# Optimization experiments

Hardware: AMD Instinct MI355X
Metric: run time of the kernel (lower is better)

Reference implementation:

```python
import jax, jax.numpy as jnp
import numpy as np

THR = 10.0           # spike threshold (all layers, igarss2023 config)
LEAK1, LEAK2, LEAK3 = 9.0, 1.0, 0.0  # subtractive leak per layer
POOL1_K, POOL1_S = 7, 6
POOL2_K, POOL2_S = 2, 2
WTA_BLOCK = 2        # local spatial WTA window


def conv2d_same(x, w):
    # x: (B,C,H,W), w: (O,I,kh,kw)
    return jax.lax.conv_general_dilated(
        x, w, window_strides=(1, 1), padding='SAME',
        dimension_numbers=('NCHW', 'OIHW', 'NCHW'))


def maxpool(x, k, s):
    return jax.lax.reduce_window(
        x, -jnp.inf, jax.lax.max, (1, 1, k, k), (1, 1, s, s), 'VALID')


def wta(mem, spk, block=WTA_BLOCK):
    """Winner-take-all lateral inhibition ('both' mode):
    (1) channel competition: only the channel with max membrane at each
        spatial location may spike; (2) local spatial competition: only the
        max-membrane neuron within each block x block window of each map
        may spike. Requires H,W divisible by block."""
    C = mem.shape[1]
    ch_win = jnp.argmax(mem, axis=1)                         # (B,H,W)
    ch_mask = jax.nn.one_hot(ch_win, C, axis=1, dtype=mem.dtype)  # (B,C,H,W)
    loc = jax.lax.reduce_window(
        mem, -jnp.inf, jax.lax.max,
        (1, 1, block, block), (1, 1, block, block), 'VALID')
    loc_up = jnp.repeat(jnp.repeat(loc, block, axis=2), block, axis=3)
    sp_mask = (mem >= loc_up).astype(mem.dtype)
    return spk * ch_mask * sp_mask


def lif_step(mem, inp, leak, use_wta):
    # integrate -> threshold -> WTA -> reset-to-zero -> subtractive leak
    mem = mem + inp
    spk = (mem >= THR).astype(mem.dtype)
    if use_wta:
        spk = wta(mem, spk)
    mem = jnp.where(spk > 0, 0.0, mem)
    mem = jnp.maximum(mem - leak, 0.0)
    return mem, spk


def setup_inputs() -> dict:
    key = jax.random.key(0)
    k0, k1, k2, k3 = jax.random.split(key, 4)
    T, B, H, W = 20, 8, 256, 256
    x = jax.random.uniform(k0, (T, B, 1, H, W), dtype=jnp.float32)
    # STDP-style weights are non-negative in [0,1)
    w1 = jax.random.uniform(k1, (4, 1, 5, 5), dtype=jnp.float32)
    w2 = jax.random.uniform(k2, (36, 4, 5, 5), dtype=jnp.float32)
    w3 = jax.random.uniform(k3, (1, 36, 7, 7), dtype=jnp.float32)
    return {"x": x, "w1": w1, "w2": w2, "w3": w3}


def reference(x, w1, w2, w3):
    T, B, _, H, W = x.shape
    H1, W1 = H, W                                   # conv1 SAME
    H2 = (H1 - POOL1_K) // POOL1_S + 1              # 42
    W2 = (W1 - POOL1_K) // POOL1_S + 1
    H3 = (H2 - POOL2_K) // POOL2_S + 1              # 21
    W3 = (W2 - POOL2_K) // POOL2_S + 1
    C1, C2, C3 = w1.shape[0], w2.shape[0], w3.shape[0]

    m1_0 = jnp.zeros((B, C1, H1, W1), x.dtype)
    m2_0 = jnp.zeros((B, C2, H2, W2), x.dtype)
    m3_0 = jnp.zeros((B, C3, H3, W3), x.dtype)

    def step(carry, xt):
        m1, m2, m3 = carry
        m1, s1 = lif_step(m1, conv2d_same(xt, w1), LEAK1, True)
        p1 = maxpool(s1, POOL1_K, POOL1_S)
        m2, s2 = lif_step(m2, conv2d_same(p1, w2), LEAK2, True)
        p2 = maxpool(s2, POOL2_K, POOL2_S)
        m3, s3 = lif_step(m3, conv2d_same(p2, w3), LEAK3, False)
        return (m1, m2, m3), s3

    _, cls_spikes = jax.lax.scan(step, (m1_0, m2_0, m3_0), x)
    return cls_spikes  # (T, B, n_classes, H3, W3)
```

## Files before the change

### kernel.cpp

```cpp
#include <hip/hip_runtime.h>
#include <stdint.h>

#define THR 10.0f
#define AGT __HIP_MEMORY_SCOPE_AGENT

static constexpr size_t OFF_P2  = 2097152;
static constexpr size_t OFF_BAR = 2359296;

static __device__ __forceinline__ uint64_t ldu64(const uint64_t* p) {
    return __hip_atomic_load(p, __ATOMIC_RELAXED, AGT);
}
static __device__ __forceinline__ void stu64(uint64_t* p, uint64_t v) {
    __hip_atomic_store(p, v, __ATOMIC_RELAXED, AGT);
}

__global__ __launch_bounds__(256) void zero_bar(uint32_t* __restrict__ bar) {
    if (threadIdx.x < 256) bar[threadIdx.x] = 0u;
}

__device__ __forceinline__ void gbar(uint32_t* bar, int bid, uint32_t n) {
    __syncthreads();
    if (threadIdx.x == 0) {
        uint32_t* base = bar + (bid >> 6) * 32;
        uint32_t a = __hip_atomic_fetch_add(base, 1u, __ATOMIC_RELAXED, AGT);
        if (a == 64u * n - 1u)
            __hip_atomic_fetch_add(base + 16, 1u, __ATOMIC_RELAXED, AGT);
        while (__hip_atomic_load(base + 16, __ATOMIC_RELAXED, AGT) < n)
            __builtin_amdgcn_s_sleep(2);
    }
    __syncthreads();
}

__global__ __launch_bounds__(256, 2) void spike_persist(
    const float* __restrict__ x,
    const float* __restrict__ w1,
    const float* __restrict__ w2,
    const float* __restrict__ w3,
    float* __restrict__ out,
    uint8_t* __restrict__ s1b,
    uint8_t* __restrict__ p2b,
    uint32_t* __restrict__ bar)
{
    __shared__ union {
        float    xs[2112];
        uint64_t st64[279];
    } u;
    __shared__ float    ps[400];
    __shared__ float    mem_s[1296];
    __shared__ float    bm_s[324];
    __shared__ int      wc_s[36];
    __shared__ uint32_t p2a[18];

    const int tid = threadIdx.x;
    const int bid = blockIdx.x;
    uint32_t nbar = 0;

    const int b1 = bid >> 6;
    const int r0 = (bid & 63) * 4;
    const int tr = tid >> 7, tc = tid & 127;

    const int tIdx = bid & 63;
    const int b2 = bid >> 6;
    const int tyi = tIdx >> 3, txi = tIdx & 7;
    const int oy2 = tyi < 5 ? 6 * tyi : 30 + 4 * (tyi - 5);
    const int ox2 = txi < 5 ? 6 * txi : 30 + 4 * (txi - 5);
    const int th2 = tyi < 5 ? 6 : 4;
    const int tw2 = txi < 5 ? 6 : 4;
    const int wave = tid >> 6, lane = tid & 63;
    const int pr = lane / 6, pc = lane - 6 * pr;
    const bool act = (pr < th2) && (pc < tw2);
    const int prA = pr > 5 ? 0 : pr, pcA = pc;

    const int lid3 = (bid & 63) * 4 + wave;
    const int kyl = lane / 7, kxl = lane % 7;

    float w3v[36];
#pragma unroll
    for (int c = 0; c < 36; c++) w3v[c] = (lane < 49) ? w3[c * 49 + lane] : 0.f;

    int aoff[9]; uint32_t avalm = 0;
#pragma unroll
    for (int i = 0; i < 9; i++) {
        int idx = tid + i * 256;
        int row = idx / 264, col = idx - row * 264;
        int gy = r0 + row - 2, gx = col - 2;
        if ((idx < 2112) && gy >= 0 && gy < 256 && gx >= 0 && gx < 256)
            avalm |= 1u << i;
        aoff[i] = gy * 256 + gx;
    }
    const int s1soff64 = (b1 * 128 + (r0 >> 1) + tr) * 32 + (tc >> 2);

    const int rb0 = 3 * oy2 - 6;
    const int cb0 = (3 * ox2 - 6) >> 1;
    const int cq0 = cb0 >> 1;
    const int d16 = 2 * (cb0 & 1);
    int boff[2]; uint32_t bvalm = 0;
#pragma unroll
    for (int i = 0; i < 2; i++) {
        int idx = tid + i * 256;
        int row = idx / 9, q = idx - 9 * row;
        int grow = rb0 + row;
        int ucol = 2 * (cq0 + q);
        if ((idx < 279) && grow >= 0 && grow < 128 && ucol >= 0 && ucol < 64)
            bvalm |= 1u << i;
        boff[i] = (b2 * 128 + grow) * 32 + cq0 + q;
    }

    bool l3in[2], l3v[2]; int l3o[2];
#pragma unroll
    for (int rep = 0; rep < 2; rep++) {
        int o = lid3 + rep * 256;
        int rr = o / 21, cl = o - rr * 21;
        int yy = rr + kyl - 3, xx = cl + kxl - 3;
        l3in[rep] = o < 441;
        l3v[rep] = (o < 441) && (lane < 49) && yy >= 0 && yy < 21 && xx >= 0 && xx < 21;
        l3o[rep] = b2 * 441 + yy * 21 + xx;
    }

    float m1r[4][2][2];
#pragma unroll
    for (int c = 0; c < 4; c++)
#pragma unroll
        for (int dy = 0; dy < 2; dy++)
#pragma unroll
            for (int dx = 0; dx < 2; dx++) m1r[c][dy][dx] = 0.f;
    float m2r[9];
#pragma unroll
    for (int i = 0; i < 9; i++) m2r[i] = 0.f;
    float m3r[2] = {0.f, 0.f};

    for (int k = 0; k < 7; k++) {
        for (int tt = 0; tt < 4; tt++) {
            const int t = 4 * k + tt;
            if (t < 20) {
                uint64_t* s1w = reinterpret_cast<uint64_t*>(s1b + (size_t)(t & 7) * 262144);
                const float* xb = x + ((size_t)t * 8 + b1) * 65536;
                __syncthreads();
#pragma unroll
                for (int i = 0; i < 9; i++) {
                    int idx = tid + i * 256;
                    if (idx < 2112) u.xs[idx] = ((avalm >> i) & 1u) ? xb[aoff[i]] : 0.f;
                }
                __syncthreads();

                const float2* xs2 = reinterpret_cast<const float2*>(u.xs);
                float p[6][6];
#pragma unroll
                for (int i = 0; i < 6; i++)
#pragma unroll
                    for (int j = 0; j < 3; j++) {
                        float2 v = xs2[(2 * tr + i) * 132 + tc + j];
                        p[i][2 * j] = v.x; p[i][2 * j + 1] = v.y;
                    }

                float acc[4][2][2];
#pragma unroll
                for (int c = 0; c < 4; c++)
#pragma unroll
                    for (int dy = 0; dy < 2; dy++)
#pragma unroll
                        for (int dx = 0; dx < 2; dx++) acc[c][dy][dx] = 0.f;
#pragma unroll
                for (int c = 0; c < 4; c++)
#pragma unroll
                    for (int ky = 0; ky < 5; ky++)
#pragma unroll
                        for (int kx = 0; kx < 5; kx++) {
                            float w = w1[c * 25 + ky * 5 + kx];
#pragma unroll
                            for (int dy = 0; dy < 2; dy++)
#pragma unroll
                                for (int dx = 0; dx < 2; dx++)
                                    acc[c][dy][dx] = fmaf(p[dy + ky][dx + kx], w, acc[c][dy][dx]);
                        }

                float mem[4][2][2];
#pragma unroll
                for (int c = 0; c < 4; c++)
#pragma unroll
                    for (int dy = 0; dy < 2; dy++)
#pragma unroll
                        for (int dx = 0; dx < 2; dx++)
                            mem[c][dy][dx] = m1r[c][dy][dx] + acc[c][dy][dx];

                int wc[2][2];
#pragma unroll
                for (int dy = 0; dy < 2; dy++)
#pragma unroll
                    for (int dx = 0; dx < 2; dx++) {
                        int w = 0; float mx = mem[0][dy][dx];
#pragma unroll
                        for (int c = 1; c < 4; c++) {
                            float v = mem[c][dy][dx];
                            if (v > mx) { mx = v; w = c; }
                        }
                        wc[dy][dx] = w;
                    }

                float bm[4];
#pragma unroll
                for (int c = 0; c < 4; c++)
                    bm[c] = fmaxf(fmaxf(mem[c][0][0], mem[c][0][1]),
                                  fmaxf(mem[c][1][0], mem[c][1][1]));

                uint32_t bits = 0;
#pragma unroll
                for (int c = 0; c < 4; c++)
#pragma unroll
                    for (int dy = 0; dy < 2; dy++)
#pragma unroll
                        for (int dx = 0; dx < 2; dx++) {
                            float m = mem[c][dy][dx];
                            bool s = (m >= THR) && (wc[dy][dx] == c) && (m >= bm[c]);
                            m1r[c][dy][dx] = fmaxf((s ? 0.f : m) - 9.0f, 0.f);
                            bits |= (s ? 1u : 0u) << (c * 4 + dy * 2 + dx);
                        }
                uint32_t b32 = bits | ((uint32_t)__shfl_xor((int)bits, 1, 64) << 16);
                uint64_t b64 = (uint64_t)b32 |
                               ((uint64_t)(uint32_t)__shfl_xor((int)b32, 2, 64) << 32);
                if (!(tid & 3)) stu64(s1w + s1soff64, b64);
            }
        }

        for (int tt = 0; tt < 4; tt++) {
            const int tl = 4 * k - 8 + tt;
            if (tl >= 0 && tl < 20) {
                const uint64_t* pb64 = reinterpret_cast<const uint64_t*>(
                    p2b + (size_t)(tl & 7) * 32768);
#pragma unroll
                for (int rep = 0; rep < 2; rep++) {
                    if (l3in[rep]) {
                        int o = lid3 + rep * 256;
                        uint64_t v = l3v[rep] ? ldu64(pb64 + l3o[rep]) : 0ull;
                        uint32_t lo = (uint32_t)v, hi = (uint32_t)(v >> 32);
                        float accv = 0.f;
#pragma unroll
                        for (int c = 0; c < 32; c++) accv += ((lo >> c) & 1u) ? w3v[c] : 0.f;
#pragma unroll
                        for (int c = 0; c < 4; c++)  accv += ((hi >> c) & 1u) ? w3v[32 + c] : 0.f;
#pragma unroll
                        for (int off = 32; off; off >>= 1) accv += __shfl_xor(accv, off, 64);
                        float memv3 = m3r[rep] + accv;
                        bool s = memv3 >= THR;
                        if (lane == 0) out[(size_t)tl * 3528 + b2 * 441 + o] = s ? 1.f : 0.f;
                        m3r[rep] = fmaxf(s ? 0.f : memv3, 0.f);
                    }
                }
            }
        }

        for (int tt = 0; tt < 4; tt++) {
            const int tb = 4 * k - 4 + tt;
            if (tb >= 0 && tb < 20) {
                const uint64_t* s1r64 = reinterpret_cast<const uint64_t*>(
                    s1b + (size_t)(tb & 7) * 262144);
                uint64_t* p2w64 = reinterpret_cast<uint64_t*>(p2b + (size_t)(tb & 7) * 32768);

                __syncthreads();
#pragma unroll
                for (int i = 0; i < 2; i++) {
                    int idx = tid + i * 256;
                    if (idx < 279)
                        u.st64[idx] = ((bvalm >> i) & 1u) ? ldu64(s1r64 + boff[i]) : 0ull;
                }
                if (tid < 18) p2a[tid] = 0;
                __syncthreads();

                if (tid < 100) {
                    int r = tid / 10, cc2 = tid - 10 * (tid / 10);
                    int gy = oy2 - 2 + r, gx = ox2 - 2 + cc2;
                    uint32_t accb = 0;
                    if (r < th2 + 4 && cc2 < tw2 + 4 && gy >= 0 && gy < 42 && gx >= 0 && gx < 42) {
                        const uint16_t* st16 = reinterpret_cast<const uint16_t*>(u.st64);
#pragma unroll
                        for (int kr = 0; kr < 4; kr++)
#pragma unroll
                            for (int kc = 0; kc < 4; kc++) {
                                uint32_t m = (kr < 3) ? (kc < 3 ? 0xFu : 0x5u)
                                                      : (kc < 3 ? 0x3u : 0x1u);
                                uint32_t v = st16[(3 * r + kr) * 36 + 3 * cc2 + kc + d16];
                                accb |= v & (m * 0x1111u);
                            }
                    }
#pragma unroll
                    for (int ic = 0; ic < 4; ic++)
                        ps[ic * 100 + tid] = ((accb >> (4 * ic)) & 0xFu) ? 1.f : 0.f;
                }
                __syncthreads();

                float pv[4][5][5];
#pragma unroll
                for (int ic = 0; ic < 4; ic++)
#pragma unroll
                    for (int i = 0; i < 5; i++)
#pragma unroll
                        for (int j = 0; j < 5; j++)
                            pv[ic][i][j] = ps[ic * 100 + (prA + i) * 10 + (pcA + j)];

                float memv[9];
                for (int cc = 0; cc < 9; cc++) {
                    int c = cc * 4 + wave;
                    const float* wr = w2 + (size_t)__builtin_amdgcn_readfirstlane(c) * 100;
                    float accv = 0.f;
#pragma unroll
                    for (int ic = 0; ic < 4; ic++)
#pragma unroll
                        for (int i = 0; i < 5; i++)
#pragma unroll
                            for (int j = 0; j < 5; j++)
                                accv = fmaf(pv[ic][i][j], wr[ic * 25 + i * 5 + j], accv);
                    float m = act ? (m2r[cc] + accv) : -1e30f;
                    memv[cc] = m;
                    if (lane < 36) mem_s[c * 36 + lane] = m;
                }
                __syncthreads();

                if (tid < 36) {
                    float mx = mem_s[tid]; int w = 0;
#pragma unroll
                    for (int c = 1; c < 36; c++) {
                        float v = mem_s[c * 36 + tid];
                        if (v > mx) { mx = v; w = c; }
                    }
                    wc_s[tid] = w;
                }
#pragma unroll
                for (int i = 0; i < 2; i++) {
                    int idx = tid + i * 256;
                    if (idx < 324) {
                        int c = idx / 9, blk = idx - 9 * c;
                        int br = blk / 3, bc2 = blk - 3 * br;
                        int l0 = 12 * br + 2 * bc2;
                        float a = mem_s[c * 36 + l0],     bb2 = mem_s[c * 36 + l0 + 1];
                        float d = mem_s[c * 36 + l0 + 6], e   = mem_s[c * 36 + l0 + 7];
                        bm_s[idx] = fmaxf(fmaxf(a, bb2), fmaxf(d, e));
                    }
                }
                __syncthreads();

                const int blkl = (pr >> 1) * 3 + (pc >> 1);
                for (int cc = 0; cc < 9; cc++) {
                    int c = cc * 4 + wave;
                    if (act) {
                        float m = memv[cc];
                        bool s = (m >= THR) && (wc_s[lane] == c) && (m >= bm_s[c * 9 + blkl]);
                        m2r[cc] = fmaxf((s ? 0.f : m) - 1.0f, 0.f);
                    }
                }

#pragma unroll
                for (int i = 0; i < 2; i++) {
                    int idx = tid + i * 256;
                    if (idx < 324) {
                        int c = idx / 9, blk = idx - 9 * c;
                        int br = blk / 3, bc2 = blk - 3 * br;
                        if (2 * br < th2 && 2 * bc2 < tw2) {
                            int l0 = 12 * br + 2 * bc2;
                            float bmv = bm_s[idx];
                            bool any = false;
#pragma unroll
                            for (int kk = 0; kk < 4; kk++) {
                                int l = l0 + (kk >> 1) * 6 + (kk & 1);
                                float m = mem_s[c * 36 + l];
                                any |= (m >= THR) && (wc_s[l] == c) && (m >= bmv);
                            }
                            if (any)
                                atomicOr(&p2a[(blk << 1) + (c >> 5)], 1u << (c & 31));
                        }
                    }
                }
                __syncthreads();

                if (tid < 9) {
                    int br = tid / 3, bc2 = tid - 3 * br;
                    if (2 * br < th2 && 2 * bc2 < tw2) {
                        int cell = b2 * 441 + ((oy2 >> 1) + br) * 21 + (ox2 >> 1) + bc2;
                        uint64_t v = (uint64_t)p2a[tid * 2] |
                                     ((uint64_t)p2a[tid * 2 + 1] << 32);
                        stu64(p2w64 + cell, v);
                    }
                }
            }
        }

        if (k < 6) gbar(bar, bid, ++nbar);
    }
}

extern "C" void kernel_launch(void* const* d_in, const int* in_sizes, int n_in,
                              void* d_out, int out_size, void* d_ws, size_t ws_size,
                              hipStream_t stream) {
    const float* x  = (const float*)d_in[0];
    const float* w1 = (const float*)d_in[1];
    const float* w2 = (const float*)d_in[2];
    const float* w3 = (const float*)d_in[3];
    float* out = (float*)d_out;
    uint8_t* s1 = (uint8_t*)d_ws;
    uint8_t* p2 = (uint8_t*)d_ws + OFF_P2;
    uint32_t* bar = (uint32_t*)((char*)d_ws + OFF_BAR);

    zero_bar<<<1, 256, 0, stream>>>(bar);

    void* args[] = {(void*)&x, (void*)&w1, (void*)&w2, (void*)&w3,
                    (void*)&out, (void*)&s1, (void*)&p2, (void*)&bar};
    hipLaunchCooperativeKernel((void*)spike_persist, dim3(512), dim3(256),
                               args, 0, stream);
}
```

Before: 398.1 us.

## Split persistent kernel into separate layer-1 and layer-2/3 block roles

Doubles the cooperative grid to 1024 blocks and gives each block one role: half compute conv1/LIF1 spikes and the other half compute conv2/WTA and layer-3. The per-batch barrier count doubles to 128 participants. The aim is to run the stages concurrently on different CUs instead of serially inside one block, trading for higher occupancy demands (a cooperative launch needs all blocks resident) and more barrier contention.

```diff
diff --git a/kernel.cpp b/kernel.cpp
--- a/kernel.cpp
+++ b/kernel.cpp
@@ -18,12 +18,12 @@
     if (threadIdx.x < 256) bar[threadIdx.x] = 0u;
 }
 
-__device__ __forceinline__ void gbar(uint32_t* bar, int bid, uint32_t n) {
+__device__ __forceinline__ void gbar(uint32_t* bar, int batch, uint32_t n) {
     __syncthreads();
     if (threadIdx.x == 0) {
-        uint32_t* base = bar + (bid >> 6) * 32;
+        uint32_t* base = bar + batch * 32;
         uint32_t a = __hip_atomic_fetch_add(base, 1u, __ATOMIC_RELAXED, AGT);
-        if (a == 64u * n - 1u)
+        if (a == 128u * n - 1u)
             __hip_atomic_fetch_add(base + 16, 1u, __ATOMIC_RELAXED, AGT);
         while (__hip_atomic_load(base + 16, __ATOMIC_RELAXED, AGT) < n)
             __builtin_amdgcn_s_sleep(2);
@@ -53,337 +53,344 @@
 
     const int tid = threadIdx.x;
     const int bid = blockIdx.x;
+    const int hi = bid >> 8;
+    const int role = hi & 1;
+    const int aidx = ((hi >> 1) << 8) | (bid & 255);
+    const int batch = aidx >> 6;
+    const int idx64 = aidx & 63;
     uint32_t nbar = 0;
 
-    const int b1 = bid >> 6;
-    const int r0 = (bid & 63) * 4;
-    const int tr = tid >> 7, tc = tid & 127;
-
-    const int tIdx = bid & 63;
-    const int b2 = bid >> 6;
-    const int tyi = tIdx >> 3, txi = tIdx & 7;
-    const int oy2 = tyi < 5 ? 6 * tyi : 30 + 4 * (tyi - 5);
-    const int ox2 = txi < 5 ? 6 * txi : 30 + 4 * (txi - 5);
-    const int th2 = tyi < 5 ? 6 : 4;
-    const int tw2 = txi < 5 ? 6 : 4;
-    const int wave = tid >> 6, lane = tid & 63;
-    const int pr = lane / 6, pc = lane - 6 * pr;
-    const bool act = (pr < th2) && (pc < tw2);
-    const int prA = pr > 5 ? 0 : pr, pcA = pc;
-
-    const int lid3 = (bid & 63) * 4 + wave;
-    const int kyl = lane / 7, kxl = lane % 7;
-
-    float w3v[36];
-#pragma unroll
-    for (int c = 0; c < 36; c++) w3v[c] = (lane < 49) ? w3[c * 49 + lane] : 0.f;
-
-    int aoff[9]; uint32_t avalm = 0;
-#pragma unroll
-    for (int i = 0; i < 9; i++) {
-        int idx = tid + i * 256;
-        int row = idx / 264, col = idx - row * 264;
-        int gy = r0 + row - 2, gx = col - 2;
-        if ((idx < 2112) && gy >= 0 && gy < 256 && gx >= 0 && gx < 256)
-            avalm |= 1u << i;
-        aoff[i] = gy * 256 + gx;
-    }
-    const int s1soff64 = (b1 * 128 + (r0 >> 1) + tr) * 32 + (tc >> 2);
-
-    const int rb0 = 3 * oy2 - 6;
-    const int cb0 = (3 * ox2 - 6) >> 1;
-    const int cq0 = cb0 >> 1;
-    const int d16 = 2 * (cb0 & 1);
-    int boff[2]; uint32_t bvalm = 0;
-#pragma unroll
-    for (int i = 0; i < 2; i++) {
-        int idx = tid + i * 256;
-        int row = idx / 9, q = idx - 9 * row;
-        int grow = rb0 + row;
-        int ucol = 2 * (cq0 + q);
-        if ((idx < 279) && grow >= 0 && grow < 128 && ucol >= 0 && ucol < 64)
-            bvalm |= 1u << i;
-        boff[i] = (b2 * 128 + grow) * 32 + cq0 + q;
-    }
-
-    bool l3in[2], l3v[2]; int l3o[2];
-#pragma unroll
-    for (int rep = 0; rep < 2; rep++) {
-        int o = lid3 + rep * 256;
-        int rr = o / 21, cl = o - rr * 21;
-        int yy = rr + kyl - 3, xx = cl + kxl - 3;
-        l3in[rep] = o < 441;
-        l3v[rep] = (o < 441) && (lane < 49) && yy >= 0 && yy < 21 && xx >= 0 && xx < 21;
-        l3o[rep] = b2 * 441 + yy * 21 + xx;
-    }
-
-    float m1r[4][2][2];
-#pragma unroll
-    for (int c = 0; c < 4; c++)
-#pragma unroll
-        for (int dy = 0; dy < 2; dy++)
-#pragma unroll
-            for (int dx = 0; dx < 2; dx++) m1r[c][dy][dx] = 0.f;
-    float m2r[9];
-#pragma unroll
-    for (int i = 0; i < 9; i++) m2r[i] = 0.f;
-    float m3r[2] = {0.f, 0.f};
-
-    for (int k = 0; k < 7; k++) {
-        for (int tt = 0; tt < 4; tt++) {
-            const int t = 4 * k + tt;
-            if (t < 20) {
-                uint64_t* s1w = reinterpret_cast<uint64_t*>(s1b + (size_t)(t & 7) * 262144);
-                const float* xb = x + ((size_t)t * 8 + b1) * 65536;
-                __syncthreads();
-#pragma unroll
-                for (int i = 0; i < 9; i++) {
-                    int idx = tid + i * 256;
-                    if (idx < 2112) u.xs[idx] = ((avalm >> i) & 1u) ? xb[aoff[i]] : 0.f;
-                }
-                __syncthreads();
-
-                const float2* xs2 = reinterpret_cast<const float2*>(u.xs);
-                float p[6][6];
-#pragma unroll
-                for (int i = 0; i < 6; i++)
-#pragma unroll
-                    for (int j = 0; j < 3; j++) {
-                        float2 v = xs2[(2 * tr + i) * 132 + tc + j];
-                        p[i][2 * j] = v.x; p[i][2 * j + 1] = v.y;
-                    }
-
-                float acc[4][2][2];
-#pragma unroll
-                for (int c = 0; c < 4; c++)
+    if (role == 0) {
+        const int r0 = idx64 * 4;
+        const int tr = tid >> 7, tc = tid & 127;
+
+        int aoff[9]; uint32_t avalm = 0;
+#pragma unroll
+        for (int i = 0; i < 9; i++) {
+            int idx = tid + i * 256;
+            int row = idx / 264, col = idx - row * 264;
+            int gy = r0 + row - 2, gx = col - 2;
+            if ((idx < 2112) && gy >= 0 && gy < 256 && gx >= 0 && gx < 256)
+                avalm |= 1u << i;
+            aoff[i] = gy * 256 + gx;
+        }
+        const int s1soff64 = (batch * 128 + (r0 >> 1) + tr) * 32 + (tc >> 2);
+
+        float m1r[4][2][2];
+#pragma unroll
+        for (int c = 0; c < 4; c++)
+#pragma unroll
+            for (int dy = 0; dy < 2; dy++)
+#pragma unroll
+                for (int dx = 0; dx < 2; dx++) m1r[c][dy][dx] = 0.f;
+
+        for (int k = 0; k < 7; k++) {
+            for (int tt = 0; tt < 4; tt++) {
+                const int t = 4 * k + tt;
+                if (t < 20) {
+                    uint64_t* s1w = reinterpret_cast<uint64_t*>(s1b + (size_t)(t & 7) * 262144);
+                    const float* xb = x + ((size_t)t * 8 + batch) * 65536;
+                    __syncthreads();
+#pragma unroll
+                    for (int i = 0; i < 9; i++) {
+                        int idx = tid + i * 256;
+                        if (idx < 2112) u.xs[idx] = ((avalm >> i) & 1u) ? xb[aoff[i]] : 0.f;
+                    }
+                    __syncthreads();
+
+                    const float2* xs2 = reinterpret_cast<const float2*>(u.xs);
+                    float p[6][6];
+#pragma unroll
+                    for (int i = 0; i < 6; i++)
+#pragma unroll
+                        for (int j = 0; j < 3; j++) {
+                            float2 v = xs2[(2 * tr + i) * 132 + tc + j];
+                            p[i][2 * j] = v.x; p[i][2 * j + 1] = v.y;
+                        }
+
+                    float acc[4][2][2];
+#pragma unroll
+                    for (int c = 0; c < 4; c++)
+#pragma unroll
+                        for (int dy = 0; dy < 2; dy++)
+#pragma unroll
+                            for (int dx = 0; dx < 2; dx++) acc[c][dy][dx] = 0.f;
+#pragma unroll
+                    for (int c = 0; c < 4; c++)
+#pragma unroll
+                        for (int ky = 0; ky < 5; ky++)
+#pragma unroll
+                            for (int kx = 0; kx < 5; kx++) {
+                                float w = w1[c * 25 + ky * 5 + kx];
+#pragma unroll
+                                for (int dy = 0; dy < 2; dy++)
+#pragma unroll
+                                    for (int dx = 0; dx < 2; dx++)
+                                        acc[c][dy][dx] = fmaf(p[dy + ky][dx + kx], w, acc[c][dy][dx]);
+                            }
+
+                    float mem[4][2][2];
+#pragma unroll
+                    for (int c = 0; c < 4; c++)
+#pragma unroll
+                        for (int dy = 0; dy < 2; dy++)
+#pragma unroll
+                            for (int dx = 0; dx < 2; dx++)
+                                mem[c][dy][dx] = m1r[c][dy][dx] + acc[c][dy][dx];
+
+                    int wc[2][2];
 #pragma unroll
                     for (int dy = 0; dy < 2; dy++)
 #pragma unroll
-                        for (int dx = 0; dx < 2; dx++) acc[c][dy][dx] = 0.f;
-#pragma unroll
-                for (int c = 0; c < 4; c++)
-#pragma unroll
-                    for (int ky = 0; ky < 5; ky++)
-#pragma unroll
-                        for (int kx = 0; kx < 5; kx++) {
-                            float w = w1[c * 25 + ky * 5 + kx];
-#pragma unroll
-                            for (int dy = 0; dy < 2; dy++)
-#pragma unroll
-                                for (int dx = 0; dx < 2; dx++)
-                                    acc[c][dy][dx] = fmaf(p[dy + ky][dx + kx], w, acc[c][dy][dx]);
-                        }
-
-                float mem[4][2][2];
-#pragma unroll
-                for (int c = 0; c < 4; c++)
-#pragma unroll
-                    for (int dy = 0; dy < 2; dy++)
-#pragma unroll
-                        for (int dx = 0; dx < 2; dx++)
-                            mem[c][dy][dx] = m1r[c][dy][dx] + acc[c][dy][dx];
-
-                int wc[2][2];
-#pragma unroll
-                for (int dy = 0; dy < 2; dy++)
-#pragma unroll
-                    for (int dx = 0; dx < 2; dx++) {
-                        int w = 0; float mx = mem[0][dy][dx];
-#pragma unroll
-                        for (int c = 1; c < 4; c++) {
-                            float v = mem[c][dy][dx];
-                            if (v > mx) { mx = v; w = c; }
-                        }
-                        wc[dy][dx] = w;
-                    }
-
-                float bm[4];
-#pragma unroll
-                for (int c = 0; c < 4; c++)
-                    bm[c] = fmaxf(fmaxf(mem[c][0][0], mem[c][0][1]),
-                                  fmaxf(mem[c][1][0], mem[c][1][1]));
-
-                uint32_t bits = 0;
-#pragma unroll
-                for (int c = 0; c < 4; c++)
-#pragma unroll
-                    for (int dy = 0; dy < 2; dy++)
-#pragma unroll
                         for (int dx = 0; dx < 2; dx++) {
-                            float m = mem[c][dy][dx];
-                            bool s = (m >= THR) && (wc[dy][dx] == c) && (m >= bm[c]);
-                            m1r[c][dy][dx] = fmaxf((s ? 0.f : m) - 9.0f, 0.f);
-                            bits |= (s ? 1u : 0u) << (c * 4 + dy * 2 + dx);
-                        }
-                uint32_t b32 = bits | ((uint32_t)__shfl_xor((int)bits, 1, 64) << 16);
-                uint64_t b64 = (uint64_t)b32 |
-                               ((uint64_t)(uint32_t)__shfl_xor((int)b32, 2, 64) << 32);
-                if (!(tid & 3)) stu64(s1w + s1soff64, b64);
-            }
-        }
-
-        for (int tt = 0; tt < 4; tt++) {
-            const int tl = 4 * k - 8 + tt;
-            if (tl >= 0 && tl < 20) {
-                const uint64_t* pb64 = reinterpret_cast<const uint64_t*>(
-                    p2b + (size_t)(tl & 7) * 32768);
-#pragma unroll
-                for (int rep = 0; rep < 2; rep++) {
-                    if (l3in[rep]) {
-                        int o = lid3 + rep * 256;
-                        uint64_t v = l3v[rep] ? ldu64(pb64 + l3o[rep]) : 0ull;
-                        uint32_t lo = (uint32_t)v, hi = (uint32_t)(v >> 32);
-                        float accv = 0.f;
-#pragma unroll
-                        for (int c = 0; c < 32; c++) accv += ((lo >> c) & 1u) ? w3v[c] : 0.f;
-#pragma unroll
-                        for (int c = 0; c < 4; c++)  accv += ((hi >> c) & 1u) ? w3v[32 + c] : 0.f;
-#pragma unroll
-                        for (int off = 32; off; off >>= 1) accv += __shfl_xor(accv, off, 64);
-                        float memv3 = m3r[rep] + accv;
-                        bool s = memv3 >= THR;
-                        if (lane == 0) out[(size_t)tl * 3528 + b2 * 441 + o] = s ? 1.f : 0.f;
-                        m3r[rep] = fmaxf(s ? 0.f : memv3, 0.f);
-                    }
+                            int w = 0; float mx = mem[0][dy][dx];
+#pragma unroll
+                            for (int c = 1; c < 4; c++) {
+                                float v = mem[c][dy][dx];
+                                if (v > mx) { mx = v; w = c; }
+                            }
+                            wc[dy][dx] = w;
+                        }
+
+                    float bm[4];
+#pragma unroll
+                    for (int c = 0; c < 4; c++)
+                        bm[c] = fmaxf(fmaxf(mem[c][0][0], mem[c][0][1]),
+                                      fmaxf(mem[c][1][0], mem[c][1][1]));
+
+                    uint32_t bits = 0;
+#pragma unroll
+                    for (int c = 0; c < 4; c++)
+#pragma unroll
+                        for (int dy = 0; dy < 2; dy++)
+#pragma unroll
+                            for (int dx = 0; dx < 2; dx++) {
+                                float m = mem[c][dy][dx];
+                                bool s = (m >= THR) && (wc[dy][dx] == c) && (m >= bm[c]);
+                                m1r[c][dy][dx] = fmaxf((s ? 0.f : m) - 9.0f, 0.f);
+                                bits |= (s ? 1u : 0u) << (c * 4 + dy * 2 + dx);
+                            }
+                    uint32_t b32 = bits | ((uint32_t)__shfl_xor((int)bits, 1, 64) << 16);
+                    uint64_t b64 = (uint64_t)b32 |
+                                   ((uint64_t)(uint32_t)__shfl_xor((int)b32, 2, 64) << 32);
+                    if (!(tid & 3)) stu64(s1w + s1soff64, b64);
                 }
             }
+            if (k < 6) gbar(bar, batch, ++nbar);
         }
-
-        for (int tt = 0; tt < 4; tt++) {
-            const int tb = 4 * k - 4 + tt;
-            if (tb >= 0 && tb < 20) {
-                const uint64_t* s1r64 = reinterpret_cast<const uint64_t*>(
-                    s1b + (size_t)(tb & 7) * 262144);
-                uint64_t* p2w64 = reinterpret_cast<uint64_t*>(p2b + (size_t)(tb & 7) * 32768);
-
-                __syncthreads();
-#pragma unroll
-                for (int i = 0; i < 2; i++) {
-                    int idx = tid + i * 256;
-                    if (idx < 279)
-                        u.st64[idx] = ((bvalm >> i) & 1u) ? ldu64(s1r64 + boff[i]) : 0ull;
-                }
-                if (tid < 18) p2a[tid] = 0;
-                __syncthreads();
-
-                if (tid < 100) {
-                    int r = tid / 10, cc2 = tid - 10 * (tid / 10);
-                    int gy = oy2 - 2 + r, gx = ox2 - 2 + cc2;
-                    uint32_t accb = 0;
-                    if (r < th2 + 4 && cc2 < tw2 + 4 && gy >= 0 && gy < 42 && gx >= 0 && gx < 42) {
-                        const uint16_t* st16 = reinterpret_cast<const uint16_t*>(u.st64);
-#pragma unroll
-                        for (int kr = 0; kr < 4; kr++)
-#pragma unroll
-                            for (int kc = 0; kc < 4; kc++) {
-                                uint32_t m = (kr < 3) ? (kc < 3 ? 0xFu : 0x5u)
-                                                      : (kc < 3 ? 0x3u : 0x1u);
-                                uint32_t v = st16[(3 * r + kr) * 36 + 3 * cc2 + kc + d16];
-                                accb |= v & (m * 0x1111u);
-                            }
-                    }
-#pragma unroll
-                    for (int ic = 0; ic < 4; ic++)
-                        ps[ic * 100 + tid] = ((accb >> (4 * ic)) & 0xFu) ? 1.f : 0.f;
-                }
-                __syncthreads();
-
-                float pv[4][5][5];
-#pragma unroll
-                for (int ic = 0; ic < 4; ic++)
-#pragma unroll
-                    for (int i = 0; i < 5; i++)
-#pragma unroll
-                        for (int j = 0; j < 5; j++)
-                            pv[ic][i][j] = ps[ic * 100 + (prA + i) * 10 + (pcA + j)];
-
-                float memv[9];
-                for (int cc = 0; cc < 9; cc++) {
-                    int c = cc * 4 + wave;
-                    const float* wr = w2 + (size_t)__builtin_amdgcn_readfirstlane(c) * 100;
-                    float accv = 0.f;
-#pragma unroll
-                    for (int ic = 0; ic < 4; ic++)
-#pragma unroll
-                        for (int i = 0; i < 5; i++)
-#pragma unroll
-                            for (int j = 0; j < 5; j++)
-                                accv = fmaf(pv[ic][i][j], wr[ic * 25 + i * 5 + j], accv);
-                    float m = act ? (m2r[cc] + accv) : -1e30f;
-                    memv[cc] = m;
-                    if (lane < 36) mem_s[c * 36 + lane] = m;
-                }
-                __syncthreads();
-
-                if (tid < 36) {
-                    float mx = mem_s[tid]; int w = 0;
-#pragma unroll
-                    for (int c = 1; c < 36; c++) {
-                        float v = mem_s[c * 36 + tid];
-                        if (v > mx) { mx = v; w = c; }
-                    }
-                    wc_s[tid] = w;
-                }
-#pragma unroll
-                for (int i = 0; i < 2; i++) {
-                    int idx = tid + i * 256;
-                    if (idx < 324) {
-                        int c = idx / 9, blk = idx - 9 * c;
-                        int br = blk / 3, bc2 = blk - 3 * br;
-                        int l0 = 12 * br + 2 * bc2;
-                        float a = mem_s[c * 36 + l0],     bb2 = mem_s[c * 36 + l0 + 1];
-                        float d = mem_s[c * 36 + l0 + 6], e   = mem_s[c * 36 + l0 + 7];
-                        bm_s[idx] = fmaxf(fmaxf(a, bb2), fmaxf(d, e));
-                    }
-                }
-                __syncthreads();
-
-                const int blkl = (pr >> 1) * 3 + (pc >> 1);
-                for (int cc = 0; cc < 9; cc++) {
-                    int c = cc * 4 + wave;
-                    if (act) {
-                        float m = memv[cc];
-                        bool s = (m >= THR) && (wc_s[lane] == c) && (m >= bm_s[c * 9 + blkl]);
-                        m2r[cc] = fmaxf((s ? 0.f : m) - 1.0f, 0.f);
-                    }
-                }
-
-#pragma unroll
-                for (int i = 0; i < 2; i++) {
-                    int idx = tid + i * 256;
-                    if (idx < 324) {
-                        int c = idx / 9, blk = idx - 9 * c;
-                        int br = blk / 3, bc2 = blk - 3 * br;
-                        if (2 * br < th2 && 2 * bc2 < tw2) {
-                            int l0 = 12 * br + 2 * bc2;
-                            float bmv = bm_s[idx];
-                            bool any = false;
-#pragma unroll
-                            for (int kk = 0; kk < 4; kk++) {
-                                int l = l0 + (kk >> 1) * 6 + (kk & 1);
-                                float m = mem_s[c * 36 + l];
-                                any |= (m >= THR) && (wc_s[l] == c) && (m >= bmv);
-                            }
-                            if (any)
-                                atomicOr(&p2a[(blk << 1) + (c >> 5)], 1u << (c & 31));
-                        }
-                    }
-                }
-                __syncthreads();
-
-                if (tid < 9) {
-                    int br = tid / 3, bc2 = tid - 3 * br;
-                    if (2 * br < th2 && 2 * bc2 < tw2) {
-                        int cell = b2 * 441 + ((oy2 >> 1) + br) * 21 + (ox2 >> 1) + bc2;
-                        uint64_t v = (uint64_t)p2a[tid * 2] |
-                                     ((uint64_t)p2a[tid * 2 + 1] << 32);
-                        stu64(p2w64 + cell, v);
+    } else {
+        const int tyi = idx64 >> 3, txi = idx64 & 7;
+        const int oy2 = tyi < 5 ? 6 * tyi : 30 + 4 * (tyi - 5);
+        const int ox2 = txi < 5 ? 6 * txi : 30 + 4 * (txi - 5);
+        const int th2 = tyi < 5 ? 6 : 4;
+        const int tw2 = txi < 5 ? 6 : 4;
+        const int wave = tid >> 6, lane = tid & 63;
+        const int pr = lane / 6, pc = lane - 6 * pr;
+        const bool act = (pr < th2) && (pc < tw2);
+        const int prA = pr > 5 ? 0 : pr, pcA = pc;
+
+        const int lid3 = idx64 * 4 + wave;
+        const int kyl = lane / 7, kxl = lane % 7;
+
+        float w3v[36];
+#pragma unroll
+        for (int c = 0; c < 36; c++) w3v[c] = (lane < 49) ? w3[c * 49 + lane] : 0.f;
+
+        const int rb0 = 3 * oy2 - 6;
+        const int cb0 = (3 * ox2 - 6) >> 1;
+        const int cq0 = cb0 >> 1;
+        const int d16 = 2 * (cb0 & 1);
+        int boff[2]; uint32_t bvalm = 0;
+#pragma unroll
+        for (int i = 0; i < 2; i++) {
+            int idx = tid + i * 256;
+            int row = idx / 9, q = idx - 9 * row;
+            int grow = rb0 + row;
+            int ucol = 2 * (cq0 + q);
+            if ((idx < 279) && grow >= 0 && grow < 128 && ucol >= 0 && ucol < 64)
+                bvalm |= 1u << i;
+            boff[i] = (batch * 128 + grow) * 32 + cq0 + q;
+        }
+
+        bool l3in[2], l3v[2]; int l3o[2];
+#pragma unroll
+        for (int rep = 0; rep < 2; rep++) {
+            int o = lid3 + rep * 256;
+            int rr = o / 21, cl = o - rr * 21;
+            int yy = rr + kyl - 3, xx = cl + kxl - 3;
+            l3in[rep] = o < 441;
+            l3v[rep] = (o < 441) && (lane < 49) && yy >= 0 && yy < 21 && xx >= 0 && xx < 21;
+            l3o[rep] = batch * 441 + yy * 21 + xx;
+        }
+
+        float m2r[9];
+#pragma unroll
+        for (int i = 0; i < 9; i++) m2r[i] = 0.f;
+        float m3r[2] = {0.f, 0.f};
+
+        for (int k = 0; k < 7; k++) {
+            for (int tt = 0; tt < 4; tt++) {
+                const int tl = 4 * k - 8 + tt;
+                if (tl >= 0 && tl < 20) {
+                    const uint64_t* pb64 = reinterpret_cast<const uint64_t*>(
+                        p2b + (size_t)(tl & 7) * 32768);
+#pragma unroll
+                    for (int rep = 0; rep < 2; rep++) {
+                        if (l3in[rep]) {
+                            int o = lid3 + rep * 256;
+                            uint64_t v = l3v[rep] ? ldu64(pb64 + l3o[rep]) : 0ull;
+                            uint32_t lo = (uint32_t)v, hi2 = (uint32_t)(v >> 32);
+                            float accv = 0.f;
+#pragma unroll
+                            for (int c = 0; c < 32; c++) accv += ((lo >> c) & 1u) ? w3v[c] : 0.f;
+#pragma unroll
+                            for (int c = 0; c < 4; c++)  accv += ((hi2 >> c) & 1u) ? w3v[32 + c] : 0.f;
+#pragma unroll
+                            for (int off = 32; off; off >>= 1) accv += __shfl_xor(accv, off, 64);
+                            float memv3 = m3r[rep] + accv;
+                            bool s = memv3 >= THR;
+                            if (lane == 0) out[(size_t)tl * 3528 + batch * 441 + o] = s ? 1.f : 0.f;
+                            m3r[rep] = fmaxf(s ? 0.f : memv3, 0.f);
+                        }
                     }
                 }
             }
+
+            for (int tt = 0; tt < 4; tt++) {
+                const int tb = 4 * k - 4 + tt;
+                if (tb >= 0 && tb < 20) {
+                    const uint64_t* s1r64 = reinterpret_cast<const uint64_t*>(
+                        s1b + (size_t)(tb & 7) * 262144);
+                    uint64_t* p2w64 = reinterpret_cast<uint64_t*>(p2b + (size_t)(tb & 7) * 32768);
+
+                    __syncthreads();
+#pragma unroll
+                    for (int i = 0; i < 2; i++) {
+                        int idx = tid + i * 256;
+                        if (idx < 279)
+                            u.st64[idx] = ((bvalm >> i) & 1u) ? ldu64(s1r64 + boff[i]) : 0ull;
+                    }
+                    if (tid < 18) p2a[tid] = 0;
+                    __syncthreads();
+
+                    if (tid < 100) {
+                        int r = tid / 10, cc2 = tid - 10 * (tid / 10);
+                        int gy = oy2 - 2 + r, gx = ox2 - 2 + cc2;
+                        uint32_t accb = 0;
+                        if (r < th2 + 4 && cc2 < tw2 + 4 && gy >= 0 && gy < 42 && gx >= 0 && gx < 42) {
+                            const uint16_t* st16 = reinterpret_cast<const uint16_t*>(u.st64);
+#pragma unroll
+                            for (int kr = 0; kr < 4; kr++)
+#pragma unroll
+                                for (int kc = 0; kc < 4; kc++) {
+                                    uint32_t m = (kr < 3) ? (kc < 3 ? 0xFu : 0x5u)
+                                                          : (kc < 3 ? 0x3u : 0x1u);
+                                    uint32_t v = st16[(3 * r + kr) * 36 + 3 * cc2 + kc + d16];
+                                    accb |= v & (m * 0x1111u);
+                                }
+                        }
+#pragma unroll
+                        for (int ic = 0; ic < 4; ic++)
+                            ps[ic * 100 + tid] = ((accb >> (4 * ic)) & 0xFu) ? 1.f : 0.f;
+                    }
+                    __syncthreads();
+
+                    float pv[4][5][5];
+#pragma unroll
+                    for (int ic = 0; ic < 4; ic++)
+#pragma unroll
+                        for (int i = 0; i < 5; i++)
+#pragma unroll
+                            for (int j = 0; j < 5; j++)
+                                pv[ic][i][j] = ps[ic * 100 + (prA + i) * 10 + (pcA + j)];
+
+                    float memv[9];
+                    for (int cc = 0; cc < 9; cc++) {
+                        int c = cc * 4 + wave;
+                        const float* wr = w2 + (size_t)__builtin_amdgcn_readfirstlane(c) * 100;
+                        float accv = 0.f;
+#pragma unroll
+                        for (int ic = 0; ic < 4; ic++)
+#pragma unroll
+                            for (int i = 0; i < 5; i++)
+#pragma unroll
+                                for (int j = 0; j < 5; j++)
+                                    accv = fmaf(pv[ic][i][j], wr[ic * 25 + i * 5 + j], accv);
+                        float m = act ? (m2r[cc] + accv) : -1e30f;
+                        memv[cc] = m;
+                        if (lane < 36) mem_s[c * 36 + lane] = m;
+                    }
+                    __syncthreads();
+
+                    if (tid < 36) {
+                        float mx = mem_s[tid]; int w = 0;
+#pragma unroll
+                        for (int c = 1; c < 36; c++) {
+                            float v = mem_s[c * 36 + tid];
+                            if (v > mx) { mx = v; w = c; }
+                        }
+                        wc_s[tid] = w;
+                    }
+#pragma unroll
+                    for (int i = 0; i < 2; i++) {
+                        int idx = tid + i * 256;
+                        if (idx < 324) {
+                            int c = idx / 9, blk = idx - 9 * c;
+                            int br = blk / 3, bc2 = blk - 3 * br;
+                            int l0 = 12 * br + 2 * bc2;
+                            float a = mem_s[c * 36 + l0],     bb2 = mem_s[c * 36 + l0 + 1];
+                            float d = mem_s[c * 36 + l0 + 6], e   = mem_s[c * 36 + l0 + 7];
+                            bm_s[idx] = fmaxf(fmaxf(a, bb2), fmaxf(d, e));
+                        }
+                    }
+                    __syncthreads();
+
+                    const int blkl = (pr >> 1) * 3 + (pc >> 1);
+                    for (int cc = 0; cc < 9; cc++) {
+                        int c = cc * 4 + wave;
+                        if (act) {
+                            float m = memv[cc];
+                            bool s = (m >= THR) && (wc_s[lane] == c) && (m >= bm_s[c * 9 + blkl]);
+                            m2r[cc] = fmaxf((s ? 0.f : m) - 1.0f, 0.f);
+                        }
+                    }
+
+#pragma unroll
+                    for (int i = 0; i < 2; i++) {
+                        int idx = tid + i * 256;
+                        if (idx < 324) {
+                            int c = idx / 9, blk = idx - 9 * c;
+                            int br = blk / 3, bc2 = blk - 3 * br;
+                            if (2 * br < th2 && 2 * bc2 < tw2) {
+                                int l0 = 12 * br + 2 * bc2;
+                                float bmv = bm_s[idx];
+                                bool any = false;
+#pragma unroll
+                                for (int kk = 0; kk < 4; kk++) {
+                                    int l = l0 + (kk >> 1) * 6 + (kk & 1);
+                                    float m = mem_s[c * 36 + l];
+                                    any |= (m >= THR) && (wc_s[l] == c) && (m >= bmv);
+                                }
+                                if (any)
+                                    atomicOr(&p2a[(blk << 1) + (c >> 5)], 1u << (c & 31));
+                            }
+                        }
+                    }
+                    __syncthreads();
+
+                    if (tid < 9) {
+                        int br = tid / 3, bc2 = tid - 3 * br;
+                        if (2 * br < th2 && 2 * bc2 < tw2) {
+                            int cell = batch * 441 + ((oy2 >> 1) + br) * 21 + (ox2 >> 1) + bc2;
+                            uint64_t v = (uint64_t)p2a[tid * 2] |
+                                         ((uint64_t)p2a[tid * 2 + 1] << 32);
+                            stu64(p2w64 + cell, v);
+                        }
+                    }
+                }
+            }
+            if (k < 6) gbar(bar, batch, ++nbar);
         }
-
-        if (k < 6) gbar(bar, bid, ++nbar);
     }
 }
 
@@ -403,6 +410,6 @@
 
     void* args[] = {(void*)&x, (void*)&w1, (void*)&w2, (void*)&w3,
                     (void*)&out, (void*)&s1, (void*)&p2, (void*)&bar};
-    hipLaunchCooperativeKernel((void*)spike_persist, dim3(512), dim3(256),
+    hipLaunchCooperativeKernel((void*)spike_persist, dim3(1024), dim3(256),
                                args, 0, stream);
 }
```

Result: slower. 518.6 us (+30.3%).
